# Kernel tuning notes

Hardware: AMD Instinct MI355X
Metric: run time of the kernel (lower is better)

## Reference

```python
import jax, jax.numpy as jnp
import numpy as np

B, C, K, H, W = 2, 8, 2048, 128, 128


def setup_inputs() -> dict:
    key = jax.random.key(0)
    k1, k2, k3 = jax.random.split(key, 3)
    image_real = jax.random.normal(k1, (B, C, H, W), dtype=jnp.float32)
    image_imag = jax.random.normal(k2, (B, C, H, W), dtype=jnp.float32)
    # k-space trajectory in radians/voxel, convention of torchkbnufft: [-pi, pi]
    kspace_traj = jax.random.uniform(
        k3, (B, C, 2, K), dtype=jnp.float32, minval=-np.pi, maxval=np.pi
    )
    return {"image_real": image_real, "image_imag": image_imag, "kspace_traj": kspace_traj}


def reference(image_real, image_imag, kspace_traj):
    """Exact type-2 non-uniform DFT (the math that the Kaiser-Bessel NUFFT
    in generate_nufft_op approximates), double-vmapped over (batch, coil).

    out[b,c,k] = sum_{x,y} image[b,c,x,y] * exp(-i*(om_x[b,c,k]*gx[x] + om_y[b,c,k]*gy[y]))
    with a centered image grid gx = x - H//2, gy = y - W//2.
    The kernel is separable in x/y, so we contract in two einsums instead of
    materializing a (B,C,K,H*W) phase matrix.
    """
    image = image_real + 1j * image_imag  # (B,C,H,W) complex64
    h, w = image.shape[-2:]
    gx = (jnp.arange(h) - h // 2).astype(jnp.float32)  # centered grid coords
    gy = (jnp.arange(w) - w // 2).astype(jnp.float32)

    om_x = kspace_traj[..., 0, :]  # (B,C,K)
    om_y = kspace_traj[..., 1, :]  # (B,C,K)

    px = jnp.exp(-1j * om_x[..., None] * gx)  # (B,C,K,H)
    py = jnp.exp(-1j * om_y[..., None] * gy)  # (B,C,K,W)

    tmp = jnp.einsum("bcxy,bcky->bckx", image, py)  # contract y first
    out = jnp.einsum("bckx,bckx->bck", tmp, px)  # (B,C,K) complex64
    return out
```

## Files before the change

kernel.cpp:

```cpp
#include <hip/hip_runtime.h>
#include <math.h>


using half8  = __attribute__((ext_vector_type(8))) _Float16;
using f32x4  = __attribute__((ext_vector_type(4))) float;

constexpr int Bn = 2, Cn = 8, Kn = 2048, Hn = 128, Wn = 128;
constexpr int BC  = Bn * Cn;
constexpr int KPW = 16;
constexpr int WPB = 4;
constexpr int KPB = KPW * WPB;
constexpr int NKS = Hn / 32;
constexpr int PSLOTS = 64 * Wn / 8;

__device__ inline void cmul(float& ar, float& ai, float br, float bi) {
    float nr = fmaf(ar, br, -ai * bi);
    ai = fmaf(ar, bi, ai * br);
    ar = nr;
}
__device__ inline void csq(float& r, float& i) {
    float nr = fmaf(r, r, -i * i);
    i = 2.f * r * i;
    r = nr;
}

template<int OUT_COMPLEX>
__global__ __launch_bounds__(256, 2)
void nufft_mfma(const float* __restrict__ img_re, const float* __restrict__ img_im,
                const float* __restrict__ traj, float* __restrict__ out)
{
    __shared__ half8 re_lds[2][PSLOTS];
    __shared__ half8 im_lds[2][PSLOTS];

    const int bc   = blockIdx.x / (Kn / KPB);
    const int kt   = blockIdx.x % (Kn / KPB);
    const int lane = threadIdx.x & 63;
    const int wave = threadIdx.x >> 6;
    const int xlo  = lane & 15;
    const int grp  = lane >> 4;
    const int kbase = kt * KPB + wave * KPW;
    const size_t ibase = (size_t)bc * Hn * Wn;

    float4 sa[4], sb[4], sd[4], se[4];

    int s_idx[4], s_j[4], s_xl[4];
    #pragma unroll
    for (int i = 0; i < 4; ++i) {
        const int s = i * 256 + (int)threadIdx.x;
        s_idx[i] = s;
        s_xl[i]  = s >> 4;
        s_j[i]   = (s & 15) ^ (s_xl[i] & 7);
    }

    auto LOADS = [&](int p) {
        #pragma unroll
        for (int i = 0; i < 4; ++i) {
            const float* gr = img_re + ibase + (size_t)(p * 64 + s_xl[i]) * Wn + s_j[i] * 8;
            const float* gi = img_im + ibase + (size_t)(p * 64 + s_xl[i]) * Wn + s_j[i] * 8;
            sa[i] = ((const float4*)gr)[0];
            sb[i] = ((const float4*)gr)[1];
            sd[i] = ((const float4*)gi)[0];
            se[i] = ((const float4*)gi)[1];
        }
    };
    auto WRITE_LDS = [&](int b) {
        #pragma unroll
        for (int i = 0; i < 4; ++i) {
            half8 hr, hi;
            hr[0]=(_Float16)sa[i].x; hr[1]=(_Float16)sa[i].y; hr[2]=(_Float16)sa[i].z; hr[3]=(_Float16)sa[i].w;
            hr[4]=(_Float16)sb[i].x; hr[5]=(_Float16)sb[i].y; hr[6]=(_Float16)sb[i].z; hr[7]=(_Float16)sb[i].w;
            hi[0]=(_Float16)sd[i].x; hi[1]=(_Float16)sd[i].y; hi[2]=(_Float16)sd[i].z; hi[3]=(_Float16)sd[i].w;
            hi[4]=(_Float16)se[i].x; hi[5]=(_Float16)se[i].y; hi[6]=(_Float16)se[i].z; hi[7]=(_Float16)se[i].w;
            re_lds[b][s_idx[i]] = hr;
            im_lds[b][s_idx[i]] = hi;
        }
    };

    LOADS(0);

    const float om_y = traj[(size_t)(bc * 2 + 1) * Kn + (kbase + xlo)];
    float s, c;
    sincosf(om_y, &s, &c);
    const float syr = c, syi = -s;
    sincosf(om_y * (float)(grp * 8 - 64), &s, &c);
    float pr = c, pi = -s;
    float t32r = syr, t32i = syi;
    #pragma unroll
    for (int q = 0; q < 5; ++q) csq(t32r, t32i);

    half8 Ar[NKS], Ai8[NKS], An[NKS];
    #pragma unroll
    for (int kk = 0; kk < NKS; ++kk) {
        float vr[8], vi[8];
        vr[0] = pr; vi[0] = pi;
        #pragma unroll
        for (int j = 1; j < 8; ++j) {
            float nr = fmaf(vr[j-1], syr, -vi[j-1] * syi);
            vi[j]    = fmaf(vr[j-1], syi,  vi[j-1] * syr);
            vr[j]    = nr;
        }
        #pragma unroll
        for (int j = 0; j < 8; ++j) {
            Ar[kk][j]  = (_Float16)vr[j];
            Ai8[kk][j] = (_Float16)vi[j];
            An[kk][j]  = (_Float16)(-vi[j]);
        }
        cmul(pr, pi, t32r, t32i);
    }

    float eqr[4], eqi[4], etr[4], eti[4];
    #pragma unroll
    for (int r = 0; r < 4; ++r) {
        const int kr = kbase + grp * 4 + r;
        const float om_x = traj[(size_t)(bc * 2 + 0) * Kn + kr];
        sincosf(om_x, &s, &c);
        float t16r = c, t16i = -s;
        sincosf(om_x * (float)(xlo - 64), &s, &c);
        eqr[r] = c; eqi[r] = -s;
        #pragma unroll
        for (int q = 0; q < 4; ++q) csq(t16r, t16i);
        etr[r] = t16r; eti[r] = t16i;
    }

    f32x4 accr[8], acci[8];
    #pragma unroll
    for (int a = 0; a < 8; ++a) { accr[a] = (f32x4)0.f; acci[a] = (f32x4)0.f; }

    WRITE_LDS(0);
    __syncthreads();

    LOADS(1);

    auto COMPUTE = [&](int p) {
        for (int kk = 0; kk < NKS; ++kk) {
            const int jx = (kk * 4 + grp) ^ (xlo & 7);
            #pragma unroll
            for (int xt = 0; xt < 4; ++xt) {
                const int slot = (xt * 16 + xlo) * 16 + jx;
                half8 br = re_lds[p][slot];
                half8 bi = im_lds[p][slot];
                const int a = p * 4 + xt;
                accr[a] = __builtin_amdgcn_mfma_f32_16x16x32_f16(Ar[kk], br, accr[a], 0, 0, 0);
                accr[a] = __builtin_amdgcn_mfma_f32_16x16x32_f16(An[kk], bi, accr[a], 0, 0, 0);
                acci[a] = __builtin_amdgcn_mfma_f32_16x16x32_f16(Ar[kk], bi, acci[a], 0, 0, 0);
                acci[a] = __builtin_amdgcn_mfma_f32_16x16x32_f16(Ai8[kk], br, acci[a], 0, 0, 0);
            }
        }
    };

    COMPUTE(0);

    WRITE_LDS(1);
    __syncthreads();

    COMPUTE(1);

    float outr[4], outi[4];
    #pragma unroll
    for (int r = 0; r < 4; ++r) {
        float qr = eqr[r], qi = eqi[r];
        const float t16r = etr[r], t16i = eti[r];
        float orr = 0.f, oii = 0.f;
        #pragma unroll
        for (int a = 0; a < 8; ++a) {
            const float tre = accr[a][r], tim = acci[a][r];
            orr = fmaf(tre, qr, orr); orr = fmaf(-tim, qi, orr);
            oii = fmaf(tre, qi, oii); oii = fmaf( tim, qr, oii);
            cmul(qr, qi, t16r, t16i);
        }
        #pragma unroll
        for (int m = 1; m < 16; m <<= 1) {
            orr += __shfl_xor(orr, m, 64);
            oii += __shfl_xor(oii, m, 64);
        }
        outr[r] = orr; outi[r] = oii;
    }

    if (xlo == 0) {
        #pragma unroll
        for (int r = 0; r < 4; ++r) {
            const int kr = kbase + grp * 4 + r;
            if (OUT_COMPLEX) {
                out[((size_t)bc * Kn + kr) * 2 + 0] = outr[r];
                out[((size_t)bc * Kn + kr) * 2 + 1] = outi[r];
            } else {
                out[(size_t)bc * Kn + kr] = outr[r];
            }
        }
    }
}

extern "C" void kernel_launch(void* const* d_in, const int* in_sizes, int n_in,
                              void* d_out, int out_size, void* d_ws, size_t ws_size,
                              hipStream_t stream) {
    const float* img_re = (const float*)d_in[0];
    const float* img_im = (const float*)d_in[1];
    const float* traj   = (const float*)d_in[2];
    float* out = (float*)d_out;

    dim3 grid(BC * (Kn / KPB));
    dim3 block(WPB * 64);
    const bool cplx = (out_size == BC * Kn * 2);

    if (cplx) hipLaunchKernelGGL((nufft_mfma<1>), grid, block, 0, stream, img_re, img_im, traj, out);
    else      hipLaunchKernelGGL((nufft_mfma<0>), grid, block, 0, stream, img_re, img_im, traj, out);
}
```

Before: 13.22 us.

## Stage whole image in LDS at once and convert with packed fp16 instructions

Replaces the two-phase, register-staged pipeline (load the half image, write it to LDS, compute while the next half loads) with a single pass. All 128 rows are loaded, converted to fp16 with cvt_pkrtz and written to one LDS buffer before the sincos setup, followed by one barrier and one compute loop over all 8 x-tiles. This drops a barrier and the staging registers and shortens conversion code. In exchange it loses the overlap of the second half's global load with compute, and the fp16 rounding mode changes to round-toward-zero, which slightly alters accuracy. LDS size is unchanged.

```diff
diff --git a/kernel.cpp b/kernel.cpp
--- a/kernel.cpp
+++ b/kernel.cpp
@@ -2,6 +2,7 @@
 #include <math.h>
 
 
+using fp16x2 = __fp16 __attribute__((ext_vector_type(2)));
 using half8  = __attribute__((ext_vector_type(8))) _Float16;
 using f32x4  = __attribute__((ext_vector_type(4))) float;
 
@@ -11,7 +12,7 @@
 constexpr int WPB = 4;
 constexpr int KPB = KPW * WPB;
 constexpr int NKS = Hn / 32;
-constexpr int PSLOTS = 64 * Wn / 8;
+constexpr int SLOTS = Hn * Wn / 8;
 
 __device__ inline void cmul(float& ar, float& ai, float br, float bi) {
     float nr = fmaf(ar, br, -ai * bi);
@@ -29,8 +30,8 @@
 void nufft_mfma(const float* __restrict__ img_re, const float* __restrict__ img_im,
                 const float* __restrict__ traj, float* __restrict__ out)
 {
-    __shared__ half8 re_lds[2][PSLOTS];
-    __shared__ half8 im_lds[2][PSLOTS];
+    __shared__ half8 re_lds[SLOTS];
+    __shared__ half8 im_lds[SLOTS];
 
     const int bc   = blockIdx.x / (Kn / KPB);
     const int kt   = blockIdx.x % (Kn / KPB);
@@ -41,42 +42,27 @@
     const int kbase = kt * KPB + wave * KPW;
     const size_t ibase = (size_t)bc * Hn * Wn;
 
-    float4 sa[4], sb[4], sd[4], se[4];
-
-    int s_idx[4], s_j[4], s_xl[4];
     #pragma unroll
-    for (int i = 0; i < 4; ++i) {
-        const int s = i * 256 + (int)threadIdx.x;
-        s_idx[i] = s;
-        s_xl[i]  = s >> 4;
-        s_j[i]   = (s & 15) ^ (s_xl[i] & 7);
+    for (int i = 0; i < 8; ++i) {
+        const int s  = i * 256 + (int)threadIdx.x;
+        const int x  = s >> 4;
+        const int j  = (s & 15) ^ (x & 7);
+        const float* gr = img_re + ibase + (size_t)x * Wn + j * 8;
+        const float* gi = img_im + ibase + (size_t)x * Wn + j * 8;
+        float4 a = ((const float4*)gr)[0], b = ((const float4*)gr)[1];
+        float4 d = ((const float4*)gi)[0], e = ((const float4*)gi)[1];
+        union { fp16x2 v2[4]; half8 v8; } ur, ui;
+        ur.v2[0] = __builtin_amdgcn_cvt_pkrtz(a.x, a.y);
+        ur.v2[1] = __builtin_amdgcn_cvt_pkrtz(a.z, a.w);
+        ur.v2[2] = __builtin_amdgcn_cvt_pkrtz(b.x, b.y);
+        ur.v2[3] = __builtin_amdgcn_cvt_pkrtz(b.z, b.w);
+        ui.v2[0] = __builtin_amdgcn_cvt_pkrtz(d.x, d.y);
+        ui.v2[1] = __builtin_amdgcn_cvt_pkrtz(d.z, d.w);
+        ui.v2[2] = __builtin_amdgcn_cvt_pkrtz(e.x, e.y);
+        ui.v2[3] = __builtin_amdgcn_cvt_pkrtz(e.z, e.w);
+        re_lds[s] = ur.v8;
+        im_lds[s] = ui.v8;
     }
-
-    auto LOADS = [&](int p) {
-        #pragma unroll
-        for (int i = 0; i < 4; ++i) {
-            const float* gr = img_re + ibase + (size_t)(p * 64 + s_xl[i]) * Wn + s_j[i] * 8;
-            const float* gi = img_im + ibase + (size_t)(p * 64 + s_xl[i]) * Wn + s_j[i] * 8;
-            sa[i] = ((const float4*)gr)[0];
-            sb[i] = ((const float4*)gr)[1];
-            sd[i] = ((const float4*)gi)[0];
-            se[i] = ((const float4*)gi)[1];
-        }
-    };
-    auto WRITE_LDS = [&](int b) {
-        #pragma unroll
-        for (int i = 0; i < 4; ++i) {
-            half8 hr, hi;
-            hr[0]=(_Float16)sa[i].x; hr[1]=(_Float16)sa[i].y; hr[2]=(_Float16)sa[i].z; hr[3]=(_Float16)sa[i].w;
-            hr[4]=(_Float16)sb[i].x; hr[5]=(_Float16)sb[i].y; hr[6]=(_Float16)sb[i].z; hr[7]=(_Float16)sb[i].w;
-            hi[0]=(_Float16)sd[i].x; hi[1]=(_Float16)sd[i].y; hi[2]=(_Float16)sd[i].z; hi[3]=(_Float16)sd[i].w;
-            hi[4]=(_Float16)se[i].x; hi[5]=(_Float16)se[i].y; hi[6]=(_Float16)se[i].z; hi[7]=(_Float16)se[i].w;
-            re_lds[b][s_idx[i]] = hr;
-            im_lds[b][s_idx[i]] = hi;
-        }
-    };
-
-    LOADS(0);
 
     const float om_y = traj[(size_t)(bc * 2 + 1) * Kn + (kbase + xlo)];
     float s, c;
@@ -126,34 +112,21 @@
     #pragma unroll
     for (int a = 0; a < 8; ++a) { accr[a] = (f32x4)0.f; acci[a] = (f32x4)0.f; }
 
-    WRITE_LDS(0);
     __syncthreads();
 
-    LOADS(1);
-
-    auto COMPUTE = [&](int p) {
-        for (int kk = 0; kk < NKS; ++kk) {
-            const int jx = (kk * 4 + grp) ^ (xlo & 7);
-            #pragma unroll
-            for (int xt = 0; xt < 4; ++xt) {
-                const int slot = (xt * 16 + xlo) * 16 + jx;
-                half8 br = re_lds[p][slot];
-                half8 bi = im_lds[p][slot];
-                const int a = p * 4 + xt;
-                accr[a] = __builtin_amdgcn_mfma_f32_16x16x32_f16(Ar[kk], br, accr[a], 0, 0, 0);
-                accr[a] = __builtin_amdgcn_mfma_f32_16x16x32_f16(An[kk], bi, accr[a], 0, 0, 0);
-                acci[a] = __builtin_amdgcn_mfma_f32_16x16x32_f16(Ar[kk], bi, acci[a], 0, 0, 0);
-                acci[a] = __builtin_amdgcn_mfma_f32_16x16x32_f16(Ai8[kk], br, acci[a], 0, 0, 0);
-            }
+    for (int kk = 0; kk < NKS; ++kk) {
+        const int jx = (kk * 4 + grp) ^ (xlo & 7);
+        #pragma unroll
+        for (int a = 0; a < 8; ++a) {
+            const int slot = (a * 16 + xlo) * 16 + jx;
+            half8 br = re_lds[slot];
+            half8 bi = im_lds[slot];
+            accr[a] = __builtin_amdgcn_mfma_f32_16x16x32_f16(Ar[kk],  br, accr[a], 0, 0, 0);
+            accr[a] = __builtin_amdgcn_mfma_f32_16x16x32_f16(An[kk],  bi, accr[a], 0, 0, 0);
+            acci[a] = __builtin_amdgcn_mfma_f32_16x16x32_f16(Ar[kk],  bi, acci[a], 0, 0, 0);
+            acci[a] = __builtin_amdgcn_mfma_f32_16x16x32_f16(Ai8[kk], br, acci[a], 0, 0, 0);
         }
-    };
-
-    COMPUTE(0);
-
-    WRITE_LDS(1);
-    __syncthreads();
-
-    COMPUTE(1);
+    }
 
     float outr[4], outi[4];
     #pragma unroll
```

New measurement: 12.69 us. 4.0% less time.
